# Performance work log

Measured on AMD Instinct MI355X. Metric: run time of the kernel, lower is better.

The kernel has to match this reference:

```python
import jax, jax.numpy as jnp
import numpy as np

SHARED_DIM = 512
ENC_IN = 512
LATENT = 16
BATCH = 65536
NUM_CLASSES = 16


def setup_inputs() -> dict:
    key = jax.random.key(0)
    ks = jax.random.split(key, 12)
    s = 1.0 / np.sqrt(SHARED_DIM)
    si = 1.0 / np.sqrt(ENC_IN)
    return {
        "x": jax.random.normal(ks[0], (BATCH, ENC_IN), dtype=jnp.float32),
        # shared MLP: two ReLU hiddens + identity output (rlkit Mlp)
        "W0": jax.random.uniform(ks[1], (SHARED_DIM, ENC_IN), jnp.float32, -si, si),
        "b0": jnp.zeros((SHARED_DIM,), jnp.float32),
        "W1": jax.random.uniform(ks[2], (SHARED_DIM, SHARED_DIM), jnp.float32, -s, s),
        "b1": jnp.zeros((SHARED_DIM,), jnp.float32),
        "W2": jax.random.uniform(ks[3], (SHARED_DIM, SHARED_DIM), jnp.float32, -s, s),
        "b2": jnp.zeros((SHARED_DIM,), jnp.float32),
        # class encoder (router)
        "Wc": jax.random.uniform(ks[4], (NUM_CLASSES, SHARED_DIM), jnp.float32, -s, s),
        "bc": jnp.zeros((NUM_CLASSES,), jnp.float32),
        # per-class gaussian experts, stacked: [K, 2*latent, shared_dim]
        "Wg": jax.random.uniform(ks[5], (NUM_CLASSES, 2 * LATENT, SHARED_DIM), jnp.float32, -s, s),
        "bg": jnp.zeros((NUM_CLASSES, 2 * LATENT), jnp.float32),
    }


def reference(x, W0, b0, W1, b1, W2, b2, Wc, bc, Wg, bg):
    # shared encoder: ReLU MLP with identity output layer
    m = jax.nn.relu(x @ W0.T + b0)
    m = jax.nn.relu(m @ W1.T + b1)
    m = m @ W2.T + b2                      # [B, D]
    # router: softmax over classes, then most-likely class per sample
    y_probs = jax.nn.softmax(m @ Wc.T + bc, axis=-1)   # [B, K]
    y = jnp.argmax(y_probs, axis=1)                    # [B]
    # evaluate ALL per-class experts densely (as the original does)
    mu_sigma = jnp.einsum('bd,ked->bke', m, Wg) + bg   # [B, K, 2L]
    mu = mu_sigma[..., :LATENT]                        # Normal mean; sampler='mean'
    # gather the selected class's mean per sample
    z = jnp.take_along_axis(mu, y[:, None, None], axis=1)[:, 0, :]  # [B, L]
    return (z, y)
```

## Files before the change

kernel.cpp:

```cpp
#include <hip/hip_runtime.h>
#include <hip/hip_bf16.h>

typedef __attribute__((ext_vector_type(8))) short short8;
typedef __attribute__((ext_vector_type(16))) float floatx16;
typedef __attribute__((ext_vector_type(4))) float floatx4;

#define AS1 __attribute__((address_space(1)))
#define AS3 __attribute__((address_space(3)))

constexpr int MM = 65536;
constexpr int KK = 512;
constexpr int NN = 512;

#define GM 128
#define GN 128
#define GK 32
#define LDT 40

__device__ __forceinline__ unsigned short bf16_rn(float v) {
  unsigned u = __float_as_uint(v);
  return (unsigned short)((u + 0x7FFFu + ((u >> 16) & 1u)) >> 16);
}
__device__ __forceinline__ float bf16_to_f32(unsigned short h) {
  return __uint_as_float((unsigned)h << 16);
}

__global__ __launch_bounds__(256) void split_kernel(
    const float* __restrict__ src, unsigned short* __restrict__ h,
    unsigned short* __restrict__ l, int n4) {
  int i = blockIdx.x * 256 + threadIdx.x;
  if (i >= n4) return;
  float4 v = ((const float4*)src)[i];
  ushort4 hv, lv;
  hv.x = bf16_rn(v.x); lv.x = bf16_rn(v.x - bf16_to_f32(hv.x));
  hv.y = bf16_rn(v.y); lv.y = bf16_rn(v.y - bf16_to_f32(hv.y));
  hv.z = bf16_rn(v.z); lv.z = bf16_rn(v.z - bf16_to_f32(hv.z));
  hv.w = bf16_rn(v.w); lv.w = bf16_rn(v.w - bf16_to_f32(hv.w));
  ((ushort4*)h)[i] = hv;
  ((ushort4*)l)[i] = lv;
}

template<bool RELU, bool SPLIT>
__global__ __launch_bounds__(256, 2) void gemm_mfma(
    const unsigned short* __restrict__ Ah, const unsigned short* __restrict__ Al,
    const unsigned short* __restrict__ Wh, const unsigned short* __restrict__ Wl,
    const float* __restrict__ bias,
    unsigned short* __restrict__ Ch, unsigned short* __restrict__ Cl,
    float* __restrict__ Cf) {
  __shared__ __align__(16) unsigned short smem[32768];
  unsigned short* sAh = smem;
  unsigned short* sAl = smem + 8192;
  unsigned short* sBh = smem + 16384;
  unsigned short* sBl = smem + 24576;
  const int tid = threadIdx.x;
  const int lane = tid & 63;
  const int wid = tid >> 6;
  const int wr = wid >> 1;
  const int wc = wid & 1;
  const int nwg = gridDim.x;
  const int hw  = blockIdx.x;
  const int logical = (hw & 7) * (nwg >> 3) + (hw >> 3);
  const int bm = logical >> 2, bn = logical & 3;
  const size_t Abase = (size_t)bm * GM * KK;
  const size_t Bbase = (size_t)bn * GN * KK;

  const unsigned short* gsrc; unsigned short* ldst; size_t tb;
  if (wid == 0)      { gsrc = Ah; tb = Abase; ldst = sAh; }
  else if (wid == 1) { gsrc = Al; tb = Abase; ldst = sAl; }
  else if (wid == 2) { gsrc = Wh; tb = Bbase; ldst = sBh; }
  else               { gsrc = Wl; tb = Bbase; ldst = sBl; }
  const int rowl = lane >> 2;
  const int gch  = (lane & 3) ^ ((lane >> 3) & 3);
  const unsigned short* gbase = gsrc + tb + (size_t)rowl * KK + gch * 8;

  auto stage = [&](int buf, int kk) {
#pragma unroll
    for (int j = 0; j < 8; ++j) {
      __builtin_amdgcn_global_load_lds(
          (const AS1 unsigned int*)(gbase + (size_t)(j * 16) * KK + kk),
          (AS3 unsigned int*)(ldst + buf * 4096 + j * 16 * GK),
          16, 0, 0);
    }
  };

  floatx16 acc[2][2];
#pragma unroll
  for (int i = 0; i < 2; ++i)
#pragma unroll
    for (int j = 0; j < 2; ++j)
#pragma unroll
      for (int r = 0; r < 16; ++r) acc[i][j][r] = 0.f;

  stage(0, 0);

  const int swz = (lane >> 1) & 3;
  int cur = 0;
#pragma unroll
  for (int k0 = 0; k0 < KK; k0 += GK) {
    if (k0 + GK < KK) {
      stage(cur ^ 1, k0 + GK);
      asm volatile("s_waitcnt vmcnt(8)" ::: "memory");
    } else {
      asm volatile("s_waitcnt vmcnt(0)" ::: "memory");
    }
    __builtin_amdgcn_s_barrier();
    __builtin_amdgcn_sched_barrier(0);

    const unsigned short* pAh = sAh + cur * 4096;
    const unsigned short* pAl = sAl + cur * 4096;
    const unsigned short* pBh = sBh + cur * 4096;
    const unsigned short* pBl = sBl + cur * 4096;
#pragma unroll
    for (int ks = 0; ks < 2; ++ks) {
      const int ch = ks * 2 + (lane >> 5);
      const int sw = (ch ^ swz) * 8;
      short8 fah[2], fal[2], fbh[2], fbl[2];
#pragma unroll
      for (int ri = 0; ri < 2; ++ri) {
        int row = wr * 64 + ri * 32 + (lane & 31);
        fah[ri] = *(const short8*)(pAh + row * GK + sw);
        fal[ri] = *(const short8*)(pAl + row * GK + sw);
      }
#pragma unroll
      for (int si = 0; si < 2; ++si) {
        int col = wc * 64 + si * 32 + (lane & 31);
        fbh[si] = *(const short8*)(pBh + col * GK + sw);
        fbl[si] = *(const short8*)(pBl + col * GK + sw);
      }
#pragma unroll
      for (int ri = 0; ri < 2; ++ri)
#pragma unroll
        for (int si = 0; si < 2; ++si) {
          acc[ri][si] = __builtin_amdgcn_mfma_f32_32x32x16_bf16(fah[ri], fbh[si], acc[ri][si], 0, 0, 0);
          acc[ri][si] = __builtin_amdgcn_mfma_f32_32x32x16_bf16(fah[ri], fbl[si], acc[ri][si], 0, 0, 0);
          acc[ri][si] = __builtin_amdgcn_mfma_f32_32x32x16_bf16(fal[ri], fbh[si], acc[ri][si], 0, 0, 0);
        }
    }
    __builtin_amdgcn_sched_barrier(0);
    __builtin_amdgcn_s_barrier();
    cur ^= 1;
  }

  if (SPLIT) {
    unsigned* lds32 = (unsigned*)smem;
#pragma unroll
    for (int si = 0; si < 2; ++si) {
      int colL = wc * 64 + si * 32 + (lane & 31);
      float bv = bias[bn * GN + colL];
#pragma unroll
      for (int ri = 0; ri < 2; ++ri) {
#pragma unroll
        for (int r = 0; r < 16; ++r) {
          int rowL = wr * 64 + ri * 32 + (r & 3) + 8 * (r >> 2) + 4 * (lane >> 5);
          float v = acc[ri][si][r] + bv;
          if (RELU) v = fmaxf(v, 0.f);
          unsigned short h = bf16_rn(v);
          unsigned short lo = bf16_rn(v - bf16_to_f32(h));
          lds32[rowL * 128 + colL] = (unsigned)h | ((unsigned)lo << 16);
        }
      }
    }
    __syncthreads();
    const int rrow = tid >> 5;
    const int rcol4 = (tid & 31) * 4;
#pragma unroll
    for (int p = 0; p < 16; ++p) {
      int row = p * 8 + rrow;
      uint4 d = *(const uint4*)&lds32[row * 128 + rcol4];
      ushort4 hv, lv;
      hv.x = (unsigned short)(d.x); lv.x = (unsigned short)(d.x >> 16);
      hv.y = (unsigned short)(d.y); lv.y = (unsigned short)(d.y >> 16);
      hv.z = (unsigned short)(d.z); lv.z = (unsigned short)(d.z >> 16);
      hv.w = (unsigned short)(d.w); lv.w = (unsigned short)(d.w >> 16);
      size_t gi = (size_t)(bm * GM + row) * NN + bn * GN + rcol4;
      *(ushort4*)&Ch[gi] = hv;
      *(ushort4*)&Cl[gi] = lv;
    }
  } else {
#pragma unroll
    for (int si = 0; si < 2; ++si) {
      int col = bn * GN + wc * 64 + si * 32 + (lane & 31);
      float bv = bias[col];
#pragma unroll
      for (int ri = 0; ri < 2; ++ri) {
#pragma unroll
        for (int r = 0; r < 16; ++r) {
          int row = bm * GM + wr * 64 + ri * 32 + (r & 3) + 8 * (r >> 2) + 4 * (lane >> 5);
          float v = acc[ri][si][r] + bv;
          if (RELU) v = fmaxf(v, 0.f);
          Cf[(size_t)row * NN + col] = v;
        }
      }
    }
  }
}

__global__ __launch_bounds__(256, 2) void gemm_muz(
    const unsigned short* __restrict__ Ahm, const unsigned short* __restrict__ Wh,
    const float* __restrict__ bias, const float* __restrict__ y_in,
    float* __restrict__ z_out) {
  __shared__ __align__(16) unsigned short smem[16384];
  unsigned short* sA = smem;
  unsigned short* sB = smem + 8192;
  const int tid = threadIdx.x;
  const int lane = tid & 63;
  const int wid = tid >> 6;
  const int wr = wid >> 1;
  const int wc = wid & 1;
  const int nwg = gridDim.x;
  const int hw  = blockIdx.x;
  const int logical = (hw & 7) * (nwg >> 3) + (hw >> 3);
  const int bm = logical >> 1, bn = logical & 1;
  const size_t Abase = (size_t)bm * GM * KK;
  const size_t Bbase = (size_t)bn * GN * KK;

  const unsigned short* gsrc = (wid < 2) ? Ahm : Wh;
  const size_t tb = (wid < 2) ? Abase : Bbase;
  unsigned short* ldst = (wid < 2) ? sA : sB;
  const int rbase = (wid & 1) * 64;
  const int rowl = lane >> 2;
  const int gch  = (lane & 3) ^ ((lane >> 3) & 3);
  const unsigned short* gbase = gsrc + tb + (size_t)rowl * KK + gch * 8;

  auto stage = [&](int buf, int kk) {
#pragma unroll
    for (int j = 0; j < 4; ++j) {
      const int r0 = rbase + j * 16;
      __builtin_amdgcn_global_load_lds(
          (const AS1 unsigned int*)(gbase + (size_t)r0 * KK + kk),
          (AS3 unsigned int*)(ldst + buf * 4096 + r0 * GK),
          16, 0, 0);
    }
  };

  floatx16 acc[2][2];
#pragma unroll
  for (int i = 0; i < 2; ++i)
#pragma unroll
    for (int j = 0; j < 2; ++j)
#pragma unroll
      for (int r = 0; r < 16; ++r) acc[i][j][r] = 0.f;

  stage(0, 0);

  const int swz = (lane >> 1) & 3;
  int cur = 0;
#pragma unroll
  for (int k0 = 0; k0 < KK; k0 += GK) {
    if (k0 + GK < KK) {
      stage(cur ^ 1, k0 + GK);
      asm volatile("s_waitcnt vmcnt(4)" ::: "memory");
    } else {
      asm volatile("s_waitcnt vmcnt(0)" ::: "memory");
    }
    __builtin_amdgcn_s_barrier();
    __builtin_amdgcn_sched_barrier(0);

    const unsigned short* pA = sA + cur * 4096;
    const unsigned short* pB = sB + cur * 4096;
#pragma unroll
    for (int ks = 0; ks < 2; ++ks) {
      const int ch = ks * 2 + (lane >> 5);
      const int sw = (ch ^ swz) * 8;
      short8 fa[2], fb[2];
#pragma unroll
      for (int ri = 0; ri < 2; ++ri) {
        int row = wr * 64 + ri * 32 + (lane & 31);
        fa[ri] = *(const short8*)(pA + row * GK + sw);
      }
#pragma unroll
      for (int si = 0; si < 2; ++si) {
        int col = wc * 64 + si * 32 + (lane & 31);
        fb[si] = *(const short8*)(pB + col * GK + sw);
      }
#pragma unroll
      for (int ri = 0; ri < 2; ++ri)
#pragma unroll
        for (int si = 0; si < 2; ++si)
          acc[ri][si] = __builtin_amdgcn_mfma_f32_32x32x16_bf16(fa[ri], fb[si], acc[ri][si], 0, 0, 0);
    }
    __builtin_amdgcn_sched_barrier(0);
    __builtin_amdgcn_s_barrier();
    cur ^= 1;
  }

  int colv[2]; float bv[2];
#pragma unroll
  for (int si = 0; si < 2; ++si) {
    colv[si] = bn * GN + wc * 64 + si * 32 + (lane & 31);
    bv[si] = bias[colv[si]];
  }
#pragma unroll
  for (int ri = 0; ri < 2; ++ri)
#pragma unroll
    for (int r = 0; r < 16; ++r) {
      int row = bm * GM + wr * 64 + ri * 32 + (r & 3) + 8 * (r >> 2) + 4 * (lane >> 5);
      int yv = (int)y_in[row];
#pragma unroll
      for (int si = 0; si < 2; ++si) {
        if ((colv[si] >> 4) == yv)
          z_out[(size_t)row * 16 + (colv[si] & 15)] = acc[ri][si][r] + bv[si];
      }
    }
}

__global__ __launch_bounds__(256) void logits_kernel(
    const unsigned short* __restrict__ mh, const unsigned short* __restrict__ ml,
    const unsigned short* __restrict__ wch, const unsigned short* __restrict__ wcl,
    const float* __restrict__ bc, float* __restrict__ y_out) {
  __shared__ unsigned short smh[64][LDT], sml[64][LDT];
  __shared__ float slog[64][17];
  const int tid = threadIdx.x;
  const int lane = tid & 63;
  const int wid = tid >> 6;
  const size_t row0 = (size_t)blockIdx.x * 64;
  const int fr = lane & 15;
  const int fq = lane >> 4;

  floatx4 acc = {0.f, 0.f, 0.f, 0.f};
  const unsigned short* bh = wch + fr * 512 + fq * 8;
  const unsigned short* bl = wcl + fr * 512 + fq * 8;

  for (int k0 = 0; k0 < 512; k0 += 32) {
    {
      int row = tid >> 2, cc = (tid & 3) * 8;
      size_t g = (row0 + row) * 512 + k0 + cc;
      *(short8*)&smh[row][cc] = *(const short8*)(mh + g);
      *(short8*)&sml[row][cc] = *(const short8*)(ml + g);
    }
    __syncthreads();
    short8 ah = *(const short8*)&smh[wid * 16 + fr][fq * 8];
    short8 al = *(const short8*)&sml[wid * 16 + fr][fq * 8];
    short8 fbh = *(const short8*)(bh + k0);
    short8 fbl = *(const short8*)(bl + k0);
    acc = __builtin_amdgcn_mfma_f32_16x16x32_bf16(ah, fbh, acc, 0, 0, 0);
    acc = __builtin_amdgcn_mfma_f32_16x16x32_bf16(ah, fbl, acc, 0, 0, 0);
    acc = __builtin_amdgcn_mfma_f32_16x16x32_bf16(al, fbh, acc, 0, 0, 0);
    __syncthreads();
  }
#pragma unroll
  for (int r = 0; r < 4; ++r)
    slog[wid * 16 + fq * 4 + r][fr] = acc[r] + bc[fr];
  __syncthreads();
  if (tid < 64) {
    float best = slog[tid][0];
    int bi = 0;
#pragma unroll
    for (int j = 1; j < 16; ++j) {
      float v = slog[tid][j];
      if (v > best) { best = v; bi = j; }
    }
    y_out[row0 + tid] = (float)bi;
  }
}

__global__ __launch_bounds__(256) void prep_wg(
    const float* __restrict__ Wg, const float* __restrict__ bg,
    unsigned short* __restrict__ wgh, float* __restrict__ wgb) {
  int gid = blockIdx.x * 256 + threadIdx.x;
  if (gid >= 32768) return;
  int r = gid >> 7;
  int c4 = (gid & 127) * 4;
  int k = r >> 4, e = r & 15;
  float4 v = *(const float4*)(Wg + ((size_t)k * 32 + e) * 512 + c4);
  ushort4 h;
  h.x = bf16_rn(v.x); h.y = bf16_rn(v.y); h.z = bf16_rn(v.z); h.w = bf16_rn(v.w);
  *(ushort4*)(wgh + (size_t)r * 512 + c4) = h;
  if (c4 == 0) wgb[r] = bg[k * 32 + e];
}

extern "C" void kernel_launch(void* const* d_in, const int* in_sizes, int n_in,
                              void* d_out, int out_size, void* d_ws, size_t ws_size,
                              hipStream_t stream) {
  const float* x  = (const float*)d_in[0];
  const float* W0 = (const float*)d_in[1];
  const float* b0 = (const float*)d_in[2];
  const float* W1 = (const float*)d_in[3];
  const float* b1 = (const float*)d_in[4];
  const float* W2 = (const float*)d_in[5];
  const float* b2 = (const float*)d_in[6];
  const float* Wc = (const float*)d_in[7];
  const float* bc = (const float*)d_in[8];
  const float* Wg = (const float*)d_in[9];
  const float* bg = (const float*)d_in[10];

  const size_t NEL = (size_t)MM * KK;
  unsigned short* Ah = (unsigned short*)d_ws;
  unsigned short* Al = Ah + NEL;
  unsigned short* Bh = Al + NEL;
  unsigned short* Bl = Bh + NEL;
  unsigned short* wch = Al;
  unsigned short* wcl = Al + 8192;
  unsigned short* wgh = Al + 16384;
  float* wgb = (float*)(Al + 16384 + 131072);

  unsigned short* w0h = (unsigned short*)d_out;
  unsigned short* w0l = w0h + 262144;
  unsigned short* w1h = w0l + 262144;
  unsigned short* w1l = w1h + 262144;
  unsigned short* w2h = w1l + 262144;
  unsigned short* w2l = w2h + 262144;

  float* z_out = (float*)d_out;
  float* y_out = z_out + (size_t)MM * 16;

  split_kernel<<<(int)(NEL / 4 / 256), 256, 0, stream>>>(x, Ah, Al, (int)(NEL / 4));
  split_kernel<<<256, 256, 0, stream>>>(W0, w0h, w0l, 65536);
  split_kernel<<<256, 256, 0, stream>>>(W1, w1h, w1l, 65536);
  split_kernel<<<256, 256, 0, stream>>>(W2, w2h, w2l, 65536);

  const int ngrid = (MM / GM) * (NN / GN);
  gemm_mfma<true , true ><<<ngrid, 256, 0, stream>>>(Ah, Al, w0h, w0l, b0, Bh, Bl, nullptr);
  gemm_mfma<true , true ><<<ngrid, 256, 0, stream>>>(Bh, Bl, w1h, w1l, b1, Ah, Al, nullptr);
  gemm_mfma<false, true ><<<ngrid, 256, 0, stream>>>(Ah, Al, w2h, w2l, b2, Bh, Bl, nullptr);

  split_kernel<<<8, 256, 0, stream>>>(Wc, wch, wcl, 2048);
  prep_wg<<<128, 256, 0, stream>>>(Wg, bg, wgh, wgb);

  logits_kernel<<<MM / 64, 256, 0, stream>>>(Bh, Bl, wch, wcl, bc, y_out);
  gemm_muz<<<(MM / GM) * 2, 256, 0, stream>>>(Bh, wgh, wgb, y_out, z_out);
}
```

Before: 660.7 us.

## Enlarge GEMM tiles to 256x256 with 8 waves and chunked epilogue

The three MLP GEMM kernels move from 128x128 tiles with 4 waves to 256x256 tiles with 8 waves (512 threads, one block per CU). Each wave now computes 128x64, which raises arithmetic intensity and halves the global traffic per output. MFMA sections are wrapped in s_setprio, and the epilogue writes through LDS in four row chunks to fit the 128KB shared buffer. The trade-off is a grid 4x smaller with one block per CU, so there is less latency hiding and more register pressure. The unused float-output path is removed.

```diff
diff --git a/kernel.cpp b/kernel.cpp
--- a/kernel.cpp
+++ b/kernel.cpp
@@ -40,52 +40,48 @@
   ((ushort4*)l)[i] = lv;
 }
 
-template<bool RELU, bool SPLIT>
-__global__ __launch_bounds__(256, 2) void gemm_mfma(
+template<bool RELU>
+__global__ __launch_bounds__(512, 1) void gemm_mfma(
     const unsigned short* __restrict__ Ah, const unsigned short* __restrict__ Al,
     const unsigned short* __restrict__ Wh, const unsigned short* __restrict__ Wl,
     const float* __restrict__ bias,
-    unsigned short* __restrict__ Ch, unsigned short* __restrict__ Cl,
-    float* __restrict__ Cf) {
-  __shared__ __align__(16) unsigned short smem[32768];
-  unsigned short* sAh = smem;
-  unsigned short* sAl = smem + 8192;
-  unsigned short* sBh = smem + 16384;
-  unsigned short* sBl = smem + 24576;
+    unsigned short* __restrict__ Ch, unsigned short* __restrict__ Cl) {
+  __shared__ __align__(16) unsigned short smem[65536];
   const int tid = threadIdx.x;
   const int lane = tid & 63;
   const int wid = tid >> 6;
-  const int wr = wid >> 1;
-  const int wc = wid & 1;
+  const int wr = wid >> 2;
+  const int wc = wid & 3;
   const int nwg = gridDim.x;
   const int hw  = blockIdx.x;
   const int logical = (hw & 7) * (nwg >> 3) + (hw >> 3);
-  const int bm = logical >> 2, bn = logical & 3;
-  const size_t Abase = (size_t)bm * GM * KK;
-  const size_t Bbase = (size_t)bn * GN * KK;
-
-  const unsigned short* gsrc; unsigned short* ldst; size_t tb;
-  if (wid == 0)      { gsrc = Ah; tb = Abase; ldst = sAh; }
-  else if (wid == 1) { gsrc = Al; tb = Abase; ldst = sAl; }
-  else if (wid == 2) { gsrc = Wh; tb = Bbase; ldst = sBh; }
-  else               { gsrc = Wl; tb = Bbase; ldst = sBl; }
+  const int bm = logical >> 1, bn = logical & 1;
+  const size_t Abase = (size_t)bm * 256 * KK;
+  const size_t Bbase = (size_t)bn * 256 * KK;
+
+  const int sarr  = wid >> 1;
+  const int rbase = (wid & 1) * 128;
+  const unsigned short* gsrc = (sarr == 0) ? Ah : (sarr == 1) ? Al
+                             : (sarr == 2) ? Wh : Wl;
+  const size_t tb = (sarr < 2) ? Abase : Bbase;
   const int rowl = lane >> 2;
   const int gch  = (lane & 3) ^ ((lane >> 3) & 3);
-  const unsigned short* gbase = gsrc + tb + (size_t)rowl * KK + gch * 8;
+  const unsigned short* gbase = gsrc + tb + (size_t)(rbase + rowl) * KK + gch * 8;
+  unsigned short* ldst = smem + sarr * 8192 + rbase * 32;
 
   auto stage = [&](int buf, int kk) {
 #pragma unroll
     for (int j = 0; j < 8; ++j) {
       __builtin_amdgcn_global_load_lds(
           (const AS1 unsigned int*)(gbase + (size_t)(j * 16) * KK + kk),
-          (AS3 unsigned int*)(ldst + buf * 4096 + j * 16 * GK),
+          (AS3 unsigned int*)(ldst + buf * 32768 + j * 16 * 32),
           16, 0, 0);
     }
   };
 
-  floatx16 acc[2][2];
-#pragma unroll
-  for (int i = 0; i < 2; ++i)
+  floatx16 acc[4][2];
+#pragma unroll
+  for (int i = 0; i < 4; ++i)
 #pragma unroll
     for (int j = 0; j < 2; ++j)
 #pragma unroll
@@ -96,9 +92,9 @@
   const int swz = (lane >> 1) & 3;
   int cur = 0;
 #pragma unroll
-  for (int k0 = 0; k0 < KK; k0 += GK) {
-    if (k0 + GK < KK) {
-      stage(cur ^ 1, k0 + GK);
+  for (int t = 0; t < 16; ++t) {
+    if (t < 15) {
+      stage(cur ^ 1, (t + 1) * GK);
       asm volatile("s_waitcnt vmcnt(8)" ::: "memory");
     } else {
       asm volatile("s_waitcnt vmcnt(0)" ::: "memory");
@@ -106,91 +102,78 @@
     __builtin_amdgcn_s_barrier();
     __builtin_amdgcn_sched_barrier(0);
 
-    const unsigned short* pAh = sAh + cur * 4096;
-    const unsigned short* pAl = sAl + cur * 4096;
-    const unsigned short* pBh = sBh + cur * 4096;
-    const unsigned short* pBl = sBl + cur * 4096;
+    const unsigned short* base = smem + cur * 32768;
 #pragma unroll
     for (int ks = 0; ks < 2; ++ks) {
       const int ch = ks * 2 + (lane >> 5);
       const int sw = (ch ^ swz) * 8;
-      short8 fah[2], fal[2], fbh[2], fbl[2];
-#pragma unroll
-      for (int ri = 0; ri < 2; ++ri) {
-        int row = wr * 64 + ri * 32 + (lane & 31);
-        fah[ri] = *(const short8*)(pAh + row * GK + sw);
-        fal[ri] = *(const short8*)(pAl + row * GK + sw);
+      short8 fah[4], fal[4], fbh[2], fbl[2];
+#pragma unroll
+      for (int ri = 0; ri < 4; ++ri) {
+        int row = wr * 128 + ri * 32 + (lane & 31);
+        fah[ri] = *(const short8*)(base + row * 32 + sw);
+        fal[ri] = *(const short8*)(base + 8192 + row * 32 + sw);
       }
 #pragma unroll
       for (int si = 0; si < 2; ++si) {
         int col = wc * 64 + si * 32 + (lane & 31);
-        fbh[si] = *(const short8*)(pBh + col * GK + sw);
-        fbl[si] = *(const short8*)(pBl + col * GK + sw);
-      }
-#pragma unroll
-      for (int ri = 0; ri < 2; ++ri)
+        fbh[si] = *(const short8*)(base + 16384 + col * 32 + sw);
+        fbl[si] = *(const short8*)(base + 24576 + col * 32 + sw);
+      }
+      __builtin_amdgcn_s_setprio(1);
+#pragma unroll
+      for (int ri = 0; ri < 4; ++ri)
 #pragma unroll
         for (int si = 0; si < 2; ++si) {
           acc[ri][si] = __builtin_amdgcn_mfma_f32_32x32x16_bf16(fah[ri], fbh[si], acc[ri][si], 0, 0, 0);
           acc[ri][si] = __builtin_amdgcn_mfma_f32_32x32x16_bf16(fah[ri], fbl[si], acc[ri][si], 0, 0, 0);
           acc[ri][si] = __builtin_amdgcn_mfma_f32_32x32x16_bf16(fal[ri], fbh[si], acc[ri][si], 0, 0, 0);
         }
+      __builtin_amdgcn_s_setprio(0);
     }
     __builtin_amdgcn_sched_barrier(0);
     __builtin_amdgcn_s_barrier();
     cur ^= 1;
   }
 
-  if (SPLIT) {
-    unsigned* lds32 = (unsigned*)smem;
+  float bv[2];
+#pragma unroll
+  for (int si = 0; si < 2; ++si)
+    bv[si] = bias[bn * 256 + wc * 64 + si * 32 + (lane & 31)];
+
+  unsigned* lds32 = (unsigned*)smem;
+#pragma unroll
+  for (int ri = 0; ri < 4; ++ri) {
+    __syncthreads();
 #pragma unroll
     for (int si = 0; si < 2; ++si) {
-      int colL = wc * 64 + si * 32 + (lane & 31);
-      float bv = bias[bn * GN + colL];
-#pragma unroll
-      for (int ri = 0; ri < 2; ++ri) {
-#pragma unroll
-        for (int r = 0; r < 16; ++r) {
-          int rowL = wr * 64 + ri * 32 + (r & 3) + 8 * (r >> 2) + 4 * (lane >> 5);
-          float v = acc[ri][si][r] + bv;
-          if (RELU) v = fmaxf(v, 0.f);
-          unsigned short h = bf16_rn(v);
-          unsigned short lo = bf16_rn(v - bf16_to_f32(h));
-          lds32[rowL * 128 + colL] = (unsigned)h | ((unsigned)lo << 16);
-        }
+      int lcol = wc * 64 + si * 32 + (lane & 31);
+#pragma unroll
+      for (int r = 0; r < 16; ++r) {
+        int frow = (r & 3) + 8 * (r >> 2) + 4 * (lane >> 5);
+        float v = acc[ri][si][r] + bv[si];
+        if (RELU) v = fmaxf(v, 0.f);
+        unsigned short h = bf16_rn(v);
+        unsigned short lo = bf16_rn(v - bf16_to_f32(h));
+        lds32[(wr * 32 + frow) * 256 + lcol] = (unsigned)h | ((unsigned)lo << 16);
       }
     }
     __syncthreads();
-    const int rrow = tid >> 5;
-    const int rcol4 = (tid & 31) * 4;
-#pragma unroll
-    for (int p = 0; p < 16; ++p) {
-      int row = p * 8 + rrow;
-      uint4 d = *(const uint4*)&lds32[row * 128 + rcol4];
+#pragma unroll
+    for (int p = 0; p < 8; ++p) {
+      int c = tid + p * 512;
+      int lrow = c >> 6;
+      int cc = (c & 63) * 4;
+      uint4 d = *(const uint4*)&lds32[lrow * 256 + cc];
       ushort4 hv, lv;
       hv.x = (unsigned short)(d.x); lv.x = (unsigned short)(d.x >> 16);
       hv.y = (unsigned short)(d.y); lv.y = (unsigned short)(d.y >> 16);
       hv.z = (unsigned short)(d.z); lv.z = (unsigned short)(d.z >> 16);
       hv.w = (unsigned short)(d.w); lv.w = (unsigned short)(d.w >> 16);
-      size_t gi = (size_t)(bm * GM + row) * NN + bn * GN + rcol4;
+      int grow = bm * 256 + (lrow >> 5) * 128 + ri * 32 + (lrow & 31);
+      size_t gi = (size_t)grow * NN + bn * 256 + cc;
       *(ushort4*)&Ch[gi] = hv;
       *(ushort4*)&Cl[gi] = lv;
-    }
-  } else {
-#pragma unroll
-    for (int si = 0; si < 2; ++si) {
-      int col = bn * GN + wc * 64 + si * 32 + (lane & 31);
-      float bv = bias[col];
-#pragma unroll
-      for (int ri = 0; ri < 2; ++ri) {
-#pragma unroll
-        for (int r = 0; r < 16; ++r) {
-          int row = bm * GM + wr * 64 + ri * 32 + (r & 3) + 8 * (r >> 2) + 4 * (lane >> 5);
-          float v = acc[ri][si][r] + bv;
-          if (RELU) v = fmaxf(v, 0.f);
-          Cf[(size_t)row * NN + col] = v;
-        }
-      }
     }
   }
 }
@@ -409,10 +392,10 @@
   split_kernel<<<256, 256, 0, stream>>>(W1, w1h, w1l, 65536);
   split_kernel<<<256, 256, 0, stream>>>(W2, w2h, w2l, 65536);
 
-  const int ngrid = (MM / GM) * (NN / GN);
-  gemm_mfma<true , true ><<<ngrid, 256, 0, stream>>>(Ah, Al, w0h, w0l, b0, Bh, Bl, nullptr);
-  gemm_mfma<true , true ><<<ngrid, 256, 0, stream>>>(Bh, Bl, w1h, w1l, b1, Ah, Al, nullptr);
-  gemm_mfma<false, true ><<<ngrid, 256, 0, stream>>>(Ah, Al, w2h, w2l, b2, Bh, Bl, nullptr);
+  const int ngrid = (MM / 256) * (NN / 256);
+  gemm_mfma<true ><<<ngrid, 512, 0, stream>>>(Ah, Al, w0h, w0l, b0, Bh, Bl);
+  gemm_mfma<true ><<<ngrid, 512, 0, stream>>>(Bh, Bl, w1h, w1l, b1, Ah, Al);
+  gemm_mfma<false><<<ngrid, 512, 0, stream>>>(Ah, Al, w2h, w2l, b2, Bh, Bl);
 
   split_kernel<<<8, 256, 0, stream>>>(Wc, wch, wcl, 2048);
   prep_wg<<<128, 256, 0, stream>>>(Wg, bg, wgh, wgb);
```

After: 624.2 us. 5.5% less time.
